# Kernel tuning notes

Hardware: AMD Instinct MI355X
Metric: run time of the kernel (lower is better)

The kernel has to match this reference:

```python
import jax, jax.numpy as jnp
import numpy as np

N_NODES = 100000
N_EDGES = 1600000
N_NODE_F = 128
N_EDGE_F = 128
N_GLOBAL_F = 64
N_GRAPHS = 256
HIDDEN = 128
IN_DIM = N_NODE_F + N_EDGE_F + N_GLOBAL_F  # 320


def setup_inputs() -> dict:
    key = jax.random.key(0)
    k1, k2, k3, k4, k5, k6 = jax.random.split(key, 6)
    node_feats = jax.random.normal(k1, (N_NODES, N_NODE_F), dtype=jnp.float32)
    edge_feats = jax.random.normal(k2, (N_EDGES, N_EDGE_F), dtype=jnp.float32)
    global_feats = jax.random.normal(k3, (N_GRAPHS, N_GLOBAL_F), dtype=jnp.float32)
    # Linear(in=320, out=128, bias=False): weight [out, in], scaled like kaiming-uniform-ish
    W = jax.random.normal(k4, (HIDDEN, IN_DIM), dtype=jnp.float32) * (1.0 / np.sqrt(IN_DIM))
    edge_index = jax.random.randint(k5, (2, N_EDGES), 0, N_NODES, dtype=jnp.int64)
    batch = jnp.sort(jax.random.randint(k6, (N_NODES,), 0, N_GRAPHS, dtype=jnp.int64))
    return {
        "node_feats": node_feats,
        "edge_feats": edge_feats,
        "global_feats": global_feats,
        "W": W,
        "edge_index": edge_index,
        "batch": batch,
    }


def reference(node_feats, edge_feats, global_feats, W, edge_index, batch):
    n_nodes = node_feats.shape[0]
    idx_dst = edge_index[1]
    # scatter-mean of edge features onto destination nodes
    sums = jax.ops.segment_sum(edge_feats, idx_dst, num_segments=n_nodes)  # [N, n_edge_f]
    counts = jax.ops.segment_sum(
        jnp.ones((edge_feats.shape[0],), dtype=edge_feats.dtype), idx_dst, num_segments=n_nodes
    )
    mean_edge = sums / jnp.maximum(counts, 1.0)[:, None]
    # concat [node, aggregated edge, gathered global]
    out = jnp.concatenate([node_feats, mean_edge, global_feats[batch]], axis=1)  # [N, 320]
    # Linear (no bias) + ShiftedSoftplus: softplus(x) - log(2)
    h = jnp.einsum("ni,oi->no", out, W)
    return jax.nn.softplus(h) - jnp.log(jnp.asarray(2.0, dtype=h.dtype))
```

## Files before the change

kernel.cpp:

```cpp
#include <hip/hip_runtime.h>
#include <math.h>

#define N_NODES   100000
#define N_EDGES   1600000
#define NODE_F    128
#define EDGE_F    128
#define GLOB_F    64
#define N_GRAPHS  256
#define HIDDEN    128
#define IN_DIM    320

#define SCAN_CHUNK 2048
#define NSCAN ((N_NODES + SCAN_CHUNK - 1) / SCAN_CHUNK)

typedef __bf16 bf16x8 __attribute__((ext_vector_type(8)));
typedef __bf16 bf16x4 __attribute__((ext_vector_type(4)));
typedef float  f32x4  __attribute__((ext_vector_type(4)));

__device__ __forceinline__ void cvt_store4(__bf16* p, float x, float y, float z, float w) {
    bf16x4 b = { (__bf16)x, (__bf16)y, (__bf16)z, (__bf16)w };
    *reinterpret_cast<bf16x4*>(p) = b;
}

__global__ __launch_bounds__(256) void wbf_kernel(const float* __restrict__ W,
                                                  __bf16* __restrict__ wbf) {
    int i = blockIdx.x * 256 + threadIdx.x;
    wbf[i] = (__bf16)W[i];
}

__global__ __launch_bounds__(256) void hist_kernel(const int* __restrict__ dst,
                                                   int* __restrict__ counts,
                                                   int* __restrict__ rank) {
    int i = blockIdx.x * 256 + threadIdx.x;
    if (i < N_EDGES) rank[i] = atomicAdd(&counts[dst[i]], 1);
}

__global__ __launch_bounds__(256) void scan1_kernel(const int* __restrict__ counts,
                                                    int* __restrict__ partial) {
    __shared__ int red[256];
    int tid = threadIdx.x;
    int base = blockIdx.x * SCAN_CHUNK + tid * 8;
    int s = 0;
    #pragma unroll
    for (int j = 0; j < 8; ++j) {
        int idx = base + j;
        if (idx < N_NODES) s += counts[idx];
    }
    red[tid] = s;
    __syncthreads();
    for (int off = 128; off > 0; off >>= 1) {
        if (tid < off) red[tid] += red[tid + off];
        __syncthreads();
    }
    if (tid == 0) partial[blockIdx.x] = red[0];
}

__global__ __launch_bounds__(64) void scan2_kernel(const int* __restrict__ partial,
                                                   int* __restrict__ pscan) {
    if (threadIdx.x == 0) {
        int run = 0;
        for (int b = 0; b < NSCAN; ++b) { pscan[b] = run; run += partial[b]; }
    }
}

__global__ __launch_bounds__(256) void scan3_kernel(const int* __restrict__ counts,
                                                    const int* __restrict__ pscan,
                                                    int* __restrict__ offs) {
    __shared__ int ts[256];
    int tid = threadIdx.x;
    int base = blockIdx.x * SCAN_CHUNK + tid * 8;
    int c[8];
    int tot = 0;
    #pragma unroll
    for (int j = 0; j < 8; ++j) {
        int idx = base + j;
        c[j] = (idx < N_NODES) ? counts[idx] : 0;
        tot += c[j];
    }
    ts[tid] = tot;
    __syncthreads();
    for (int off = 1; off < 256; off <<= 1) {
        int v = 0;
        if (tid >= off) v = ts[tid - off];
        __syncthreads();
        if (tid >= off) ts[tid] += v;
        __syncthreads();
    }
    int run = pscan[blockIdx.x] + ts[tid] - tot;
    #pragma unroll
    for (int j = 0; j < 8; ++j) {
        int idx = base + j;
        if (idx < N_NODES) { offs[idx] = run; run += c[j]; }
    }
    if (blockIdx.x == 0 && tid == 0) offs[N_NODES] = N_EDGES;
}

__global__ __launch_bounds__(256) void fill_kernel(const int* __restrict__ dst,
                                                   const int* __restrict__ rank,
                                                   const int* __restrict__ offs,
                                                   int* __restrict__ eid) {
    int i = blockIdx.x * 256 + threadIdx.x;
    if (i < N_EDGES) {
        int d = dst[i];
        eid[offs[d] + rank[i]] = i;
    }
}

__global__ __launch_bounds__(256, 6) void gather_kernel(
    const float* __restrict__ edge_feats,
    const int*   __restrict__ offs,
    const int*   __restrict__ eid,
    __bf16* __restrict__ mean_bf)
{
    const int tid  = threadIdx.x;
    const int lane = tid & 63;
    const int gl   = lane & 15;
    const int n    = blockIdx.x * 16 + (tid >> 4);

    const int beg = offs[n], end = offs[n + 1];
    const int E   = end - beg;
    const int lim = max(end - 1, 0);
    int ev = eid[min(beg + gl, lim)];

    float a0=0.f,a1=0.f,a2=0.f,a3=0.f,a4=0.f,a5=0.f,a6=0.f,a7=0.f;
    for (int c0 = 0; c0 < E; c0 += 16) {
        #pragma unroll
        for (int i = 0; i < 16; ++i) {
            int e = __shfl(ev, (lane & 48) + i);
            if (c0 + i < E) {
                const f32x4* p = reinterpret_cast<const f32x4*>(
                    edge_feats + (size_t)e * EDGE_F + gl * 8);
                f32x4 u0 = p[0];
                f32x4 u1 = p[1];
                a0 += u0.x; a1 += u0.y; a2 += u0.z; a3 += u0.w;
                a4 += u1.x; a5 += u1.y; a6 += u1.z; a7 += u1.w;
            }
        }
        ev = eid[min(beg + c0 + 16 + gl, lim)];
    }
    float ic = 1.0f / fmaxf((float)E, 1.0f);
    bf16x8 b;
    b[0]=(__bf16)(a0*ic); b[1]=(__bf16)(a1*ic);
    b[2]=(__bf16)(a2*ic); b[3]=(__bf16)(a3*ic);
    b[4]=(__bf16)(a4*ic); b[5]=(__bf16)(a5*ic);
    b[6]=(__bf16)(a6*ic); b[7]=(__bf16)(a7*ic);
    *reinterpret_cast<bf16x8*>(mean_bf + (size_t)n * EDGE_F + gl * 8) = b;
}

#define ROWS 32
#define XSTR (IN_DIM + 8)

__global__ __launch_bounds__(256) void gemm_kernel(
    const float* __restrict__ node_feats,
    const __bf16* __restrict__ mean_bf,
    const float* __restrict__ glob,
    const int*   __restrict__ batch,
    const __bf16* __restrict__ wbf,
    float* __restrict__ out)
{
    __shared__ __bf16 xs[ROWS * XSTR];

    const int tid  = threadIdx.x;
    const int row0 = blockIdx.x * ROWS;
    const int wv   = tid >> 6;
    const int lane = tid & 63;

    #pragma unroll
    for (int it = 0; it < 4; ++it) {
        int i = tid + it * 256;
        int r = i >> 5, k4 = i & 31;
        float4 v = *reinterpret_cast<const float4*>(
            node_feats + (size_t)(row0 + r) * NODE_F + k4 * 4);
        cvt_store4(&xs[r * XSTR + k4 * 4], v.x, v.y, v.z, v.w);
    }
    #pragma unroll
    for (int it = 0; it < 2; ++it) {
        int i = tid + it * 256;
        int r = i >> 4, c = i & 15;
        bf16x8 v = *reinterpret_cast<const bf16x8*>(
            mean_bf + (size_t)(row0 + r) * EDGE_F + c * 8);
        *reinterpret_cast<bf16x8*>(&xs[r * XSTR + NODE_F + c * 8]) = v;
    }
    #pragma unroll
    for (int it = 0; it < 2; ++it) {
        int i = tid + it * 256;
        int r = i >> 4, k4 = i & 15;
        int b = batch[row0 + r];
        float4 v = *reinterpret_cast<const float4*>(
            glob + (size_t)b * GLOB_F + k4 * 4);
        cvt_store4(&xs[r * XSTR + NODE_F + EDGE_F + k4 * 4], v.x, v.y, v.z, v.w);
    }

    __syncthreads();

    f32x4 acc00 = {0.f, 0.f, 0.f, 0.f};
    f32x4 acc10 = {0.f, 0.f, 0.f, 0.f};
    f32x4 acc01 = {0.f, 0.f, 0.f, 0.f};
    f32x4 acc11 = {0.f, 0.f, 0.f, 0.f};

    const int lr = lane & 15;
    const int kb = lane >> 4;

    const __bf16* wrow0 = wbf + (size_t)(wv * 32 + lr) * IN_DIM + kb * 8;
    const __bf16* wrow1 = wrow0 + 16 * IN_DIM;

    #pragma unroll 2
    for (int kt = 0; kt < IN_DIM / 32; ++kt) {
        bf16x8 a0 = *reinterpret_cast<const bf16x8*>(&xs[lr * XSTR + kt * 32 + kb * 8]);
        bf16x8 a1 = *reinterpret_cast<const bf16x8*>(&xs[(16 + lr) * XSTR + kt * 32 + kb * 8]);
        bf16x8 b0 = *reinterpret_cast<const bf16x8*>(wrow0 + kt * 32);
        bf16x8 b1 = *reinterpret_cast<const bf16x8*>(wrow1 + kt * 32);

        acc00 = __builtin_amdgcn_mfma_f32_16x16x32_bf16(a0, b0, acc00, 0, 0, 0);
        acc10 = __builtin_amdgcn_mfma_f32_16x16x32_bf16(a1, b0, acc10, 0, 0, 0);
        acc01 = __builtin_amdgcn_mfma_f32_16x16x32_bf16(a0, b1, acc01, 0, 0, 0);
        acc11 = __builtin_amdgcn_mfma_f32_16x16x32_bf16(a1, b1, acc11, 0, 0, 0);
    }

    const float LN2 = 0.69314718055994530942f;
#define EMIT(ACC, RT, CT)                                                      \
    do {                                                                       \
        int col = (wv * 2 + (CT)) * 16 + lr;                                   \
        _Pragma("unroll")                                                      \
        for (int q = 0; q < 4; ++q) {                                          \
            int row = row0 + (RT) * 16 + kb * 4 + q;                           \
            float h = ACC[q];                                                  \
            float sp = fmaxf(h, 0.f) + log1pf(__expf(-fabsf(h)));              \
            out[(size_t)row * HIDDEN + col] = sp - LN2;                        \
        }                                                                      \
    } while (0)
    EMIT(acc00, 0, 0);
    EMIT(acc10, 1, 0);
    EMIT(acc01, 0, 1);
    EMIT(acc11, 1, 1);
#undef EMIT
}

extern "C" void kernel_launch(void* const* d_in, const int* in_sizes, int n_in,
                              void* d_out, int out_size, void* d_ws, size_t ws_size,
                              hipStream_t stream) {
    const float* node_feats = (const float*)d_in[0];
    const float* edge_feats = (const float*)d_in[1];
    const float* glob       = (const float*)d_in[2];
    const float* W          = (const float*)d_in[3];
    const int*   edge_index = (const int*)d_in[4];
    const int*   batch      = (const int*)d_in[5];
    float* out = (float*)d_out;

    const int* dst = edge_index + N_EDGES;

    __bf16* wbf     = (__bf16*)d_ws;
    __bf16* mean_bf = (__bf16*)((char*)d_ws + 81920);
    int* ws_i       = (int*)((char*)d_ws + 81920 + 25600000);
    int* counts  = ws_i;
    int* partial = ws_i + 100000;
    int* pscan   = ws_i + 100064;
    int* offs    = ws_i + 100128;
    int* eid     = ws_i + 200132;
    int* rank    = ws_i + 1800132;

    hipMemsetAsync(counts, 0, (size_t)N_NODES * sizeof(int), stream);

    wbf_kernel<<<160, 256, 0, stream>>>(W, wbf);
    hist_kernel<<<N_EDGES / 256, 256, 0, stream>>>(dst, counts, rank);
    scan1_kernel<<<NSCAN, 256, 0, stream>>>(counts, partial);
    scan2_kernel<<<1, 64, 0, stream>>>(partial, pscan);
    scan3_kernel<<<NSCAN, 256, 0, stream>>>(counts, pscan, offs);
    fill_kernel<<<N_EDGES / 256, 256, 0, stream>>>(dst, rank, offs, eid);

    gather_kernel<<<N_NODES / 16, 256, 0, stream>>>(edge_feats, offs, eid, mean_bf);

    gemm_kernel<<<N_NODES / ROWS, 256, 0, stream>>>(
        node_feats, mean_bf, glob, batch, wbf, out);
}
```

Measured before the change: 349.8 us.

## Use atomic cursors for CSR fill and widen gather to 32 lanes per node

The CSR build no longer stores a per-edge rank array. The fill kernel instead claims slots with atomics on a cursor array that the scan initialises, which removes a 6.4MB write and read at the cost of a second round of atomics. The gather kernel now gives each node 32 lanes with one 16-byte load each, instead of 16 lanes with two loads. That means 8 nodes per block and raised occupancy bounds, trading per-lane work for more parallelism. Edge order within a segment becomes nondeterministic, which can change float summation order slightly.

```diff
diff --git a/kernel.cpp b/kernel.cpp
--- a/kernel.cpp
+++ b/kernel.cpp
@@ -29,10 +29,9 @@
 }
 
 __global__ __launch_bounds__(256) void hist_kernel(const int* __restrict__ dst,
-                                                   int* __restrict__ counts,
-                                                   int* __restrict__ rank) {
+                                                   int* __restrict__ counts) {
     int i = blockIdx.x * 256 + threadIdx.x;
-    if (i < N_EDGES) rank[i] = atomicAdd(&counts[dst[i]], 1);
+    if (i < N_EDGES) atomicAdd(&counts[dst[i]], 1);
 }
 
 __global__ __launch_bounds__(256) void scan1_kernel(const int* __restrict__ counts,
@@ -65,7 +64,8 @@
 
 __global__ __launch_bounds__(256) void scan3_kernel(const int* __restrict__ counts,
                                                     const int* __restrict__ pscan,
-                                                    int* __restrict__ offs) {
+                                                    int* __restrict__ offs,
+                                                    int* __restrict__ cursor) {
     __shared__ int ts[256];
     int tid = threadIdx.x;
     int base = blockIdx.x * SCAN_CHUNK + tid * 8;
@@ -90,23 +90,23 @@
     #pragma unroll
     for (int j = 0; j < 8; ++j) {
         int idx = base + j;
-        if (idx < N_NODES) { offs[idx] = run; run += c[j]; }
+        if (idx < N_NODES) { offs[idx] = run; cursor[idx] = run; run += c[j]; }
     }
     if (blockIdx.x == 0 && tid == 0) offs[N_NODES] = N_EDGES;
 }
 
 __global__ __launch_bounds__(256) void fill_kernel(const int* __restrict__ dst,
-                                                   const int* __restrict__ rank,
-                                                   const int* __restrict__ offs,
+                                                   int* __restrict__ cursor,
                                                    int* __restrict__ eid) {
     int i = blockIdx.x * 256 + threadIdx.x;
     if (i < N_EDGES) {
         int d = dst[i];
-        eid[offs[d] + rank[i]] = i;
-    }
-}
-
-__global__ __launch_bounds__(256, 6) void gather_kernel(
+        int pos = atomicAdd(&cursor[d], 1);
+        eid[pos] = i;
+    }
+}
+
+__global__ __launch_bounds__(256, 8) void gather_kernel(
     const float* __restrict__ edge_feats,
     const int*   __restrict__ offs,
     const int*   __restrict__ eid,
@@ -114,37 +114,33 @@
 {
     const int tid  = threadIdx.x;
     const int lane = tid & 63;
-    const int gl   = lane & 15;
-    const int n    = blockIdx.x * 16 + (tid >> 4);
+    const int g32  = lane & 31;
+    const int base = lane & 32;
+    const int n    = blockIdx.x * 8 + (tid >> 5);
 
     const int beg = offs[n], end = offs[n + 1];
     const int E   = end - beg;
     const int lim = max(end - 1, 0);
-    int ev = eid[min(beg + gl, lim)];
-
-    float a0=0.f,a1=0.f,a2=0.f,a3=0.f,a4=0.f,a5=0.f,a6=0.f,a7=0.f;
-    for (int c0 = 0; c0 < E; c0 += 16) {
+    int ev = eid[min(beg + g32, lim)];
+
+    float a0 = 0.f, a1 = 0.f, a2 = 0.f, a3 = 0.f;
+    for (int c0 = 0; c0 < E; c0 += 32) {
         #pragma unroll
-        for (int i = 0; i < 16; ++i) {
-            int e = __shfl(ev, (lane & 48) + i);
+        for (int i = 0; i < 32; ++i) {
+            int e = __shfl(ev, base + i);
             if (c0 + i < E) {
-                const f32x4* p = reinterpret_cast<const f32x4*>(
-                    edge_feats + (size_t)e * EDGE_F + gl * 8);
-                f32x4 u0 = p[0];
-                f32x4 u1 = p[1];
-                a0 += u0.x; a1 += u0.y; a2 += u0.z; a3 += u0.w;
-                a4 += u1.x; a5 += u1.y; a6 += u1.z; a7 += u1.w;
+                f32x4 u = *reinterpret_cast<const f32x4*>(
+                    edge_feats + (size_t)e * EDGE_F + g32 * 4);
+                a0 += u.x; a1 += u.y; a2 += u.z; a3 += u.w;
             }
         }
-        ev = eid[min(beg + c0 + 16 + gl, lim)];
+        ev = eid[min(beg + c0 + 32 + g32, lim)];
     }
     float ic = 1.0f / fmaxf((float)E, 1.0f);
-    bf16x8 b;
-    b[0]=(__bf16)(a0*ic); b[1]=(__bf16)(a1*ic);
-    b[2]=(__bf16)(a2*ic); b[3]=(__bf16)(a3*ic);
-    b[4]=(__bf16)(a4*ic); b[5]=(__bf16)(a5*ic);
-    b[6]=(__bf16)(a6*ic); b[7]=(__bf16)(a7*ic);
-    *reinterpret_cast<bf16x8*>(mean_bf + (size_t)n * EDGE_F + gl * 8) = b;
+    bf16x4 b;
+    b[0] = (__bf16)(a0 * ic); b[1] = (__bf16)(a1 * ic);
+    b[2] = (__bf16)(a2 * ic); b[3] = (__bf16)(a3 * ic);
+    *reinterpret_cast<bf16x4*>(mean_bf + (size_t)n * EDGE_F + g32 * 4) = b;
 }
 
 #define ROWS 32
@@ -256,19 +252,19 @@
     int* partial = ws_i + 100000;
     int* pscan   = ws_i + 100064;
     int* offs    = ws_i + 100128;
-    int* eid     = ws_i + 200132;
-    int* rank    = ws_i + 1800132;
+    int* cursor  = ws_i + 200132;
+    int* eid     = ws_i + 300132;
 
     hipMemsetAsync(counts, 0, (size_t)N_NODES * sizeof(int), stream);
 
     wbf_kernel<<<160, 256, 0, stream>>>(W, wbf);
-    hist_kernel<<<N_EDGES / 256, 256, 0, stream>>>(dst, counts, rank);
+    hist_kernel<<<N_EDGES / 256, 256, 0, stream>>>(dst, counts);
     scan1_kernel<<<NSCAN, 256, 0, stream>>>(counts, partial);
     scan2_kernel<<<1, 64, 0, stream>>>(partial, pscan);
-    scan3_kernel<<<NSCAN, 256, 0, stream>>>(counts, pscan, offs);
-    fill_kernel<<<N_EDGES / 256, 256, 0, stream>>>(dst, rank, offs, eid);
-
-    gather_kernel<<<N_NODES / 16, 256, 0, stream>>>(edge_feats, offs, eid, mean_bf);
+    scan3_kernel<<<NSCAN, 256, 0, stream>>>(counts, pscan, offs, cursor);
+    fill_kernel<<<N_EDGES / 256, 256, 0, stream>>>(dst, cursor, eid);
+
+    gather_kernel<<<N_NODES / 8, 256, 0, stream>>>(edge_feats, offs, eid, mean_bf);
 
     gemm_kernel<<<N_NODES / ROWS, 256, 0, stream>>>(
         node_feats, mean_bf, glob, batch, wbf, out);
```

Result: slower. 452.5 us (+29.3%).
